# Kernel optimization log

Hardware: AMD Instinct MI355X
Metric: run time of the kernel (lower is better)

## Reference

```python
import jax, jax.numpy as jnp
import numpy as np

D_MODEL = 1024
N_HEADS = 16
HEAD_DIM = 64
SEQ = 2048
BATCH = 2
NEG = -1e9


def rotate_half(t):
    t1, t2 = jnp.split(t, 2, axis=-1)
    return jnp.concatenate([-t2, t1], axis=-1)


def setup_inputs() -> dict:
    key = jax.random.key(0)
    ks = jax.random.split(key, 7)
    std = 0.02
    x = jax.random.normal(ks[0], (BATCH, SEQ, D_MODEL), dtype=jnp.float32)
    # RoPE tables [seq_len, head_dim]
    inv_freq = 1.0 / (10000.0 ** (jnp.arange(0, HEAD_DIM, 2, dtype=jnp.float32) / HEAD_DIM))
    t = jnp.arange(SEQ, dtype=jnp.float32)
    freqs = jnp.outer(t, inv_freq)
    emb = jnp.concatenate([freqs, freqs], axis=-1)
    cos = jnp.cos(emb)
    sin = jnp.sin(emb)
    Wq = std * jax.random.normal(ks[1], (D_MODEL, D_MODEL), dtype=jnp.float32)
    Wk = std * jax.random.normal(ks[2], (D_MODEL, D_MODEL), dtype=jnp.float32)
    Wv = std * jax.random.normal(ks[3], (D_MODEL, D_MODEL), dtype=jnp.float32)
    Wo = std * jax.random.normal(ks[4], (D_MODEL, D_MODEL), dtype=jnp.float32)
    return {"x": x, "cos": cos, "sin": sin, "Wq": Wq, "Wk": Wk, "Wv": Wv, "Wo": Wo}


def reference(x, cos, sin, Wq, Wk, Wv, Wo):
    B, S, _ = x.shape
    scale = 1.0 / np.sqrt(HEAD_DIM)
    # projections (nn.Linear: y = x @ W.T)
    q = (x @ Wq.T).reshape(B, S, N_HEADS, HEAD_DIM).transpose(0, 2, 1, 3)  # [B,H,S,D]
    k = (x @ Wk.T).reshape(B, S, N_HEADS, HEAD_DIM).transpose(0, 2, 1, 3)
    v = (x @ Wv.T).reshape(B, S, N_HEADS, HEAD_DIM).transpose(0, 2, 1, 3)
    # RoPE
    c = cos[None, None, :, :]
    s = sin[None, None, :, :]
    q = q * c + rotate_half(q) * s
    k = k * c + rotate_half(k) * s
    # attention with additive causal mask
    scores = jnp.einsum('bhqd,bhkd->bhqk', q, k) * scale
    causal = jnp.triu(jnp.ones((S, S), dtype=jnp.float32), k=1) * NEG
    scores = scores + causal[None, None]
    attn = jax.nn.softmax(scores, axis=-1)
    out = jnp.einsum('bhqk,bhkd->bhqd', attn, v)
    out = out.transpose(0, 2, 1, 3).reshape(B, S, D_MODEL)
    return out @ Wo.T
```

## Files before the change

### kernel.cpp

```cpp
#include <hip/hip_runtime.h>
#include <hip/hip_bf16.h>
#include <math.h>

#define DM    1024
#define SEQL  2048
#define NB    2
#define MTOT  4096

typedef __attribute__((ext_vector_type(8))) short short8;
typedef __attribute__((ext_vector_type(4))) short short4v;
typedef __attribute__((ext_vector_type(4))) float float4v;

#define GLDS16(g, l) __builtin_amdgcn_global_load_lds( \
    (const __attribute__((address_space(1))) void*)(g), \
    (__attribute__((address_space(3))) void*)(l), 16, 0, 0)

__device__ __forceinline__ short f2bf(float f) {
  union { float f; unsigned u; } c; c.f = f;
  unsigned r = c.u + 0x7FFFu + ((c.u >> 16) & 1u);
  return (short)(r >> 16);
}

__device__ __forceinline__ int packbf(float a, float b) {
  union { float f; unsigned u; } ca, cb; ca.f = a; cb.f = b;
  return (int)__builtin_amdgcn_perm(cb.u + 0x8000u, ca.u + 0x8000u, 0x07060302u);
}

__global__ __launch_bounds__(256) void cvt_all(
    const float* __restrict__ x, const float* __restrict__ wq, const float* __restrict__ wk,
    const float* __restrict__ wv, const float* __restrict__ wo,
    short* __restrict__ xb, short* __restrict__ wqb, short* __restrict__ wkb,
    short* __restrict__ wvb, short* __restrict__ wob) {
  const int n4x = MTOT * DM / 4;
  int i = blockIdx.x * 256 + threadIdx.x;
  const float* s; short* d; int off;
  if (i < n4x) { s = x; d = xb; off = i; }
  else {
    int j = i - n4x;
    int sel = j >> 18;
    off = j & 0x3FFFF;
    s = (sel == 0) ? wq : (sel == 1) ? wk : (sel == 2) ? wv : wo;
    d = (sel == 0) ? wqb : (sel == 1) ? wkb : (sel == 2) ? wvb : wob;
  }
  float4 v = ((const float4*)s)[off];
  short4v o;
  o.x = f2bf(v.x); o.y = f2bf(v.y); o.z = f2bf(v.z); o.w = f2bf(v.w);
  ((short4v*)d)[off] = o;
}

__global__ __launch_bounds__(256, 3) void qkv_kernel(
    const short* __restrict__ A,
    const short* __restrict__ B0, const short* __restrict__ B1, const short* __restrict__ B2,
    short* __restrict__ out0, short* __restrict__ out1, short* __restrict__ out2,
    const float* __restrict__ cosp, const float* __restrict__ sinp)
{
  __shared__ short As[2][128 * 32];
  __shared__ short Bs[2][128 * 32];
  const int t = threadIdx.x;
  const int w = t >> 6, lane = t & 63;
  const int quad = lane >> 4, l16 = lane & 15;
  const int wm = w >> 1, wn = w & 1;
  const int bm = blockIdx.y * 128, bn = blockIdx.x * 128;

  const short* Bw = (blockIdx.z == 0) ? B0 : ((blockIdx.z == 1) ? B1 : B2);

  float4v acc[4][4];
#pragma unroll
  for (int i = 0; i < 4; ++i)
#pragma unroll
    for (int j = 0; j < 4; ++j) { float4v z = {0.f, 0.f, 0.f, 0.f}; acc[i][j] = z; }

  const int srow = t >> 2, skc = t & 3;
  auto stage = [&](int k0, int p) {
#pragma unroll
    for (int i = 0; i < 2; ++i) {
      const int row = (i * 256 + t) >> 2, kc = (i * 256 + t) & 3;
      GLDS16(A  + (size_t)(bm + row) * DM + k0 + kc * 8, &As[p][(i * 256 + w * 64) * 8]);
      GLDS16(Bw + (size_t)(bn + row) * DM + k0 + kc * 8, &Bs[p][(i * 256 + w * 64) * 8]);
    }
  };
  (void)srow; (void)skc;

  stage(0, 0);
  for (int ki = 0; ki < 32; ++ki) {
    const int p = ki & 1;
    __syncthreads();
    if (ki < 31) stage((ki + 1) * 32, p ^ 1);
    short8 af[4], bf[4];
#pragma unroll
    for (int mt = 0; mt < 4; ++mt) af[mt] = *(const short8*)&As[p][(wm * 64 + mt * 16 + l16) * 32 + quad * 8];
#pragma unroll
    for (int nt = 0; nt < 4; ++nt) bf[nt] = *(const short8*)&Bs[p][(wn * 64 + nt * 16 + l16) * 32 + quad * 8];
#pragma unroll
    for (int mt = 0; mt < 4; ++mt)
#pragma unroll
      for (int nt = 0; nt < 4; ++nt)
        acc[mt][nt] = __builtin_amdgcn_mfma_f32_16x16x32_bf16(af[mt], bf[nt], acc[mt][nt], 0, 0, 0);
  }

  if (blockIdx.z < 2) {
    short* qo = (blockIdx.z == 0) ? out0 : out1;
    const float sc = (blockIdx.z == 0) ? 0.18033688011112042f : 1.0f;
#pragma unroll
    for (int mt = 0; mt < 4; ++mt)
#pragma unroll
      for (int r = 0; r < 4; ++r) {
        int grow = bm + wm * 64 + mt * 16 + quad * 4 + r;
        int s = grow & (SEQL - 1);
        int base = grow * DM + bn + wn * 64;
#pragma unroll
        for (int nt = 0; nt < 2; ++nt) {
          int d1 = nt * 16 + l16;
          float q1 = acc[mt][nt][r], q2 = acc[mt][nt + 2][r];
          float c1 = cosp[s * 64 + d1] * sc,      s1 = sinp[s * 64 + d1] * sc;
          float c2 = cosp[s * 64 + 32 + d1] * sc, s2 = sinp[s * 64 + 32 + d1] * sc;
          qo[base + d1]      = f2bf(q1 * c1 - q2 * s1);
          qo[base + 32 + d1] = f2bf(q2 * c2 + q1 * s2);
        }
      }
  } else {
    short* vo = out2;
#pragma unroll
    for (int mt = 0; mt < 4; ++mt)
#pragma unroll
      for (int nt = 0; nt < 4; ++nt) {
        int gc = bn + wn * 64 + nt * 16 + l16;
        int g0 = bm + wm * 64 + mt * 16 + quad * 4;
        short4v pk;
#pragma unroll
        for (int r = 0; r < 4; ++r) pk[r] = f2bf(acc[mt][nt][r]);
        *(short4v*)&vo[(size_t)gc * MTOT + g0] = pk;
      }
  }
}

#if __has_builtin(__builtin_amdgcn_mfma_f32_16x16x16bf16_1k)
#define HAVE_MFMA16 1
#define MFMA16(a, b, c) __builtin_amdgcn_mfma_f32_16x16x16bf16_1k(a, b, c, 0, 0, 0)
#else
#define HAVE_MFMA16 0
#endif

__global__ __launch_bounds__(256, 2) void attn_kernel(
    const short* __restrict__ Q, const short* __restrict__ K,
    const short* __restrict__ Vt, short* __restrict__ O)
{
  __shared__ short Ks[2][128 * 64];
  __shared__ short Vs[2][64 * 128];
  const int t = threadIdx.x;
  const int w = t >> 6, lane = t & 63;
  const int quad = lane >> 4, l16 = lane & 15;
  const int qtA = blockIdx.x;
  const int qtB = 31 - blockIdx.x;
  const int bh = blockIdx.y;
  const int b = bh >> 4, h = bh & 15;
  const int rowbase = b * SEQL;
  const int colbase = h * 64;
  const int nktA = (qtA >> 1) + 1;
  const int nktB = (qtB >> 1) + 1;
  const int qA = qtA * 64 + w * 16 + l16;
  const int qB = qtB * 64 + w * 16 + l16;

  short8 aqA[2], aqB[2];
#pragma unroll
  for (int kk = 0; kk < 2; ++kk) {
    aqA[kk] = *(const short8*)&Q[(size_t)(rowbase + qA) * DM + colbase + kk * 32 + quad * 8];
    aqB[kk] = *(const short8*)&Q[(size_t)(rowbase + qB) * DM + colbase + kk * 32 + quad * 8];
  }

  float4v odA[4], odB[4];
#pragma unroll
  for (int j = 0; j < 4; ++j) { float4v z = {0.f, 0.f, 0.f, 0.f}; odA[j] = z; odB[j] = z; }
  float lA = 0.f, lB = 0.f;

  auto stage = [&](int kt, int p) {
    const short* Kbase = K + (size_t)(rowbase + kt * 128) * DM + colbase;
    const short* Vbase = Vt + (size_t)colbase * MTOT + rowbase + kt * 128;
    short* kd = &Ks[p][0];
    short* vd = &Vs[p][0];
#pragma unroll
    for (int j = 0; j < 4; ++j) {
      int i = j * 256 + t;
      int n = i >> 3, c = (i & 7) ^ (n & 7);
      GLDS16(Kbase + (size_t)n * DM + c * 8, kd + (j * 256 + w * 64) * 8);
    }
#pragma unroll
    for (int j = 0; j < 4; ++j) {
      int i = j * 256 + t;
      int d = i >> 4, c = (i & 15) ^ (d & 7);
      GLDS16(Vbase + (size_t)d * MTOT + c * 8, vd + (j * 256 + w * 64) * 8);
    }
  };

  stage(0, 0);
  for (int kt = 0; kt < nktB; ++kt) {
    const int p = kt & 1;
    __syncthreads();
    if (kt + 1 < nktB) stage(kt + 1, p ^ 1);
    const short* ks = &Ks[p][0];
    const short* vs = &Vs[p][0];
    const bool actA = (kt < nktA);
    const bool diagA = (kt == nktA - 1), diagB = (kt == nktB - 1);

    int pkA[8][2], pkB[8][2];
#pragma unroll
    for (int nt = 0; nt < 8; ++nt) {
      int n = nt * 16 + l16;
      short8 bk0 = *(const short8*)&ks[(n * 8 + (quad ^ (n & 7))) * 8];
      short8 bk1 = *(const short8*)&ks[(n * 8 + ((4 + quad) ^ (n & 7))) * 8];
      const int kb = kt * 128 + nt * 16 + quad * 4;
      float4v zz = {0.f, 0.f, 0.f, 0.f};
      float4v sB = __builtin_amdgcn_mfma_f32_16x16x32_bf16(bk0, aqB[0], zz, 0, 0, 0);
      sB = __builtin_amdgcn_mfma_f32_16x16x32_bf16(bk1, aqB[1], sB, 0, 0, 0);
      float pb[4];
#pragma unroll
      for (int r = 0; r < 4; ++r) {
        float pv = (diagB && (kb + r > qB)) ? 0.f : __builtin_amdgcn_exp2f(sB[r]);
        lB += pv; pb[r] = pv;
      }
      pkB[nt][0] = packbf(pb[0], pb[1]);
      pkB[nt][1] = packbf(pb[2], pb[3]);
      if (actA) {
        float4v sA = __builtin_amdgcn_mfma_f32_16x16x32_bf16(bk0, aqA[0], zz, 0, 0, 0);
        sA = __builtin_amdgcn_mfma_f32_16x16x32_bf16(bk1, aqA[1], sA, 0, 0, 0);
        float pa[4];
#pragma unroll
        for (int r = 0; r < 4; ++r) {
          float pv = (diagA && (kb + r > qA)) ? 0.f : __builtin_amdgcn_exp2f(sA[r]);
          lA += pv; pa[r] = pv;
        }
        pkA[nt][0] = packbf(pa[0], pa[1]);
        pkA[nt][1] = packbf(pa[2], pa[3]);
      }
    }

#if HAVE_MFMA16
#pragma unroll
    for (int kk = 0; kk < 8; ++kk) {
      union { int i[2]; short4v s; } ubB, ubA;
      ubB.i[0] = pkB[kk][0]; ubB.i[1] = pkB[kk][1];
      if (actA) { ubA.i[0] = pkA[kk][0]; ubA.i[1] = pkA[kk][1]; }
#pragma unroll
      for (int dt = 0; dt < 4; ++dt) {
        int d = dt * 16 + l16;
        short4v av = *(const short4v*)&vs[(d * 16 + ((kk * 2 + (quad >> 1)) ^ (d & 7))) * 8 + (quad & 1) * 4];
        odB[dt] = MFMA16(av, ubB.s, odB[dt]);
        if (actA) odA[dt] = MFMA16(av, ubA.s, odA[dt]);
      }
    }
#else
#pragma unroll
    for (int kk = 0; kk < 4; ++kk) {
      union { int i[4]; short8 s; } ubB, ubA;
#pragma unroll
      for (int dj = 0; dj < 4; ++dj) {
        int src = (((quad & 1) * 2 + (dj >> 1)) << 4) + l16;
        int b0 = __shfl(pkB[2 * kk][dj & 1], src);
        int b1 = __shfl(pkB[2 * kk + 1][dj & 1], src);
        ubB.i[dj] = (quad >= 2) ? b1 : b0;
        int a0 = __shfl(pkA[2 * kk][dj & 1], src);
        int a1 = __shfl(pkA[2 * kk + 1][dj & 1], src);
        ubA.i[dj] = (quad >= 2) ? a1 : a0;
      }
#pragma unroll
      for (int dt = 0; dt < 4; ++dt) {
        int d = dt * 16 + l16;
        short8 av = *(const short8*)&vs[(d * 16 + ((kk * 4 + quad) ^ (d & 7))) * 8];
        odB[dt] = __builtin_amdgcn_mfma_f32_16x16x32_bf16(av, ubB.s, odB[dt], 0, 0, 0);
        if (actA) odA[dt] = __builtin_amdgcn_mfma_f32_16x16x32_bf16(av, ubA.s, odA[dt], 0, 0, 0);
      }
    }
#endif
  }

  lA += __shfl_xor(lA, 16); lA += __shfl_xor(lA, 32);
  lB += __shfl_xor(lB, 16); lB += __shfl_xor(lB, 32);
  const float iA = 1.f / lA, iB = 1.f / lB;

#pragma unroll
  for (int dt = 0; dt < 4; ++dt) {
    short4v sa, sb;
#pragma unroll
    for (int r = 0; r < 4; ++r) { sa[r] = f2bf(odA[dt][r] * iA); sb[r] = f2bf(odB[dt][r] * iB); }
    int col = colbase + dt * 16 + quad * 4;
    *(short4v*)&O[(size_t)(rowbase + qA) * DM + col] = sa;
    *(short4v*)&O[(size_t)(rowbase + qB) * DM + col] = sb;
  }
}

__global__ __launch_bounds__(256, 2) void gemm_out(
    const short* __restrict__ A, const short* __restrict__ B,
    float* __restrict__ out)
{
  __shared__ short As[2][128 * 32];
  __shared__ short Bs[2][64 * 32];
  const int t = threadIdx.x;
  const int w = t >> 6, lane = t & 63;
  const int quad = lane >> 4, l16 = lane & 15;
  const int wm = w >> 1, wn = w & 1;
  const int bm = blockIdx.y * 128, bn = blockIdx.x * 64;

  float4v acc[4][2];
#pragma unroll
  for (int i = 0; i < 4; ++i)
#pragma unroll
    for (int j = 0; j < 2; ++j) { float4v z = {0.f, 0.f, 0.f, 0.f}; acc[i][j] = z; }

  auto stage = [&](int k0, int p) {
#pragma unroll
    for (int i = 0; i < 2; ++i) {
      const int row = (i * 256 + t) >> 2, kc = (i * 256 + t) & 3;
      GLDS16(A + (size_t)(bm + row) * DM + k0 + kc * 8, &As[p][(i * 256 + w * 64) * 8]);
    }
    {
      const int row = t >> 2, kc = t & 3;
      GLDS16(B + (size_t)(bn + row) * DM + k0 + kc * 8, &Bs[p][(w * 64) * 8]);
    }
  };

  stage(0, 0);
  for (int ki = 0; ki < 32; ++ki) {
    const int p = ki & 1;
    __syncthreads();
    if (ki < 31) stage((ki + 1) * 32, p ^ 1);
    short8 af[4], bf[2];
#pragma unroll
    for (int mt = 0; mt < 4; ++mt) af[mt] = *(const short8*)&As[p][(wm * 64 + mt * 16 + l16) * 32 + quad * 8];
#pragma unroll
    for (int nt = 0; nt < 2; ++nt) bf[nt] = *(const short8*)&Bs[p][(wn * 32 + nt * 16 + l16) * 32 + quad * 8];
#pragma unroll
    for (int mt = 0; mt < 4; ++mt)
#pragma unroll
      for (int nt = 0; nt < 2; ++nt)
        acc[mt][nt] = __builtin_amdgcn_mfma_f32_16x16x32_bf16(af[mt], bf[nt], acc[mt][nt], 0, 0, 0);
  }

#pragma unroll
  for (int mt = 0; mt < 4; ++mt)
#pragma unroll
    for (int nt = 0; nt < 2; ++nt)
#pragma unroll
      for (int r = 0; r < 4; ++r) {
        int grow = bm + wm * 64 + mt * 16 + quad * 4 + r;
        int gcol = bn + wn * 32 + nt * 16 + l16;
        out[(size_t)grow * DM + gcol] = acc[mt][nt][r];
      }
}

extern "C" void kernel_launch(void* const* d_in, const int* in_sizes, int n_in,
                              void* d_out, int out_size, void* d_ws, size_t ws_size,
                              hipStream_t stream) {
  const float* x    = (const float*)d_in[0];
  const float* cosp = (const float*)d_in[1];
  const float* sinp = (const float*)d_in[2];
  const float* Wq   = (const float*)d_in[3];
  const float* Wk   = (const float*)d_in[4];
  const float* Wv   = (const float*)d_in[5];
  const float* Wo   = (const float*)d_in[6];

  char* ws = (char*)d_ws;
  const size_t XB = (size_t)MTOT * DM * 2;
  const size_t WB = (size_t)DM * DM * 2;
  short* xb    = (short*)(ws);
  short* wqb   = (short*)(ws + XB);
  short* wkb   = (short*)(ws + XB + 1 * WB);
  short* wvb   = (short*)(ws + XB + 2 * WB);
  short* wob   = (short*)(ws + XB + 3 * WB);
  short* Qb    = (short*)(ws + XB + 4 * WB);
  short* Kb    = (short*)(ws + XB + 4 * WB + XB);
  short* Vtb   = (short*)(ws + XB + 4 * WB + 2 * XB);
  short* attnb = xb;

  const int n4tot = (MTOT * DM + 4 * DM * DM) / 4;
  hipLaunchKernelGGL(cvt_all, dim3(n4tot / 256), dim3(256), 0, stream,
                     x, Wq, Wk, Wv, Wo, xb, wqb, wkb, wvb, wob);

  hipLaunchKernelGGL(qkv_kernel, dim3(DM / 128, MTOT / 128, 3), dim3(256), 0, stream,
                     xb, wqb, wkb, wvb, Qb, Kb, Vtb, cosp, sinp);

  hipLaunchKernelGGL(attn_kernel, dim3(16, NB * 16), dim3(256), 0, stream,
                     Qb, Kb, Vtb, attnb);

  hipLaunchKernelGGL(gemm_out, dim3(DM / 64, MTOT / 128), dim3(256), 0, stream,
                     attnb, wob, (float*)d_out);
}
```

Before: 201.3 us.

## Split attention key tiles across two wave groups with LDS P staging and reduction

The attention kernel now runs 512 threads per block. Two groups of four waves each handle half of every 128-key tile, and their partial outputs and row sums are combined through shared memory at the end. The probability tile is written to LDS so the PV product can use 16x16x32 MFMA with P as the A operand, replacing the register-resident packing. K/V double buffering is dropped in favour of single-buffered loads with two barriers per iteration. This is meant to raise parallelism per block, at the cost of losing load/compute overlap, extra LDS traffic and scalar bf16 output stores.

```diff
diff --git a/kernel.cpp b/kernel.cpp
--- a/kernel.cpp
+++ b/kernel.cpp
@@ -70,7 +70,6 @@
 #pragma unroll
     for (int j = 0; j < 4; ++j) { float4v z = {0.f, 0.f, 0.f, 0.f}; acc[i][j] = z; }
 
-  const int srow = t >> 2, skc = t & 3;
   auto stage = [&](int k0, int p) {
 #pragma unroll
     for (int i = 0; i < 2; ++i) {
@@ -79,7 +78,6 @@
       GLDS16(Bw + (size_t)(bn + row) * DM + k0 + kc * 8, &Bs[p][(i * 256 + w * 64) * 8]);
     }
   };
-  (void)srow; (void)skc;
 
   stage(0, 0);
   for (int ki = 0; ki < 32; ++ki) {
@@ -134,32 +132,25 @@
   }
 }
 
-#if __has_builtin(__builtin_amdgcn_mfma_f32_16x16x16bf16_1k)
-#define HAVE_MFMA16 1
-#define MFMA16(a, b, c) __builtin_amdgcn_mfma_f32_16x16x16bf16_1k(a, b, c, 0, 0, 0)
-#else
-#define HAVE_MFMA16 0
-#endif
-
-__global__ __launch_bounds__(256, 2) void attn_kernel(
+__global__ __launch_bounds__(512, 4) void attn_kernel(
     const short* __restrict__ Q, const short* __restrict__ K,
     const short* __restrict__ Vt, short* __restrict__ O)
 {
-  __shared__ short Ks[2][128 * 64];
-  __shared__ short Vs[2][64 * 128];
+  __shared__ short smem[34816];
+  short* Ks = smem;
+  short* Vs = smem + 8192;
   const int t = threadIdx.x;
-  const int w = t >> 6, lane = t & 63;
+  const int wid = t >> 6, lane = t & 63;
   const int quad = lane >> 4, l16 = lane & 15;
-  const int qtA = blockIdx.x;
-  const int qtB = 31 - blockIdx.x;
-  const int bh = blockIdx.y;
-  const int b = bh >> 4, h = bh & 15;
-  const int rowbase = b * SEQL;
-  const int colbase = h * 64;
-  const int nktA = (qtA >> 1) + 1;
-  const int nktB = (qtB >> 1) + 1;
-  const int qA = qtA * 64 + w * 16 + l16;
-  const int qB = qtB * 64 + w * 16 + l16;
+  const int g = wid >> 2;
+  const int qg = wid & 3;
+  short* Pl = smem + 16384 + wid * (2 * 16 * 72);
+  const int qtA = blockIdx.x, qtB = 31 - blockIdx.x;
+  const int bh = blockIdx.y, b = bh >> 4, h = bh & 15;
+  const int rowbase = b * SEQL, colbase = h * 64;
+  const int nktA = (qtA >> 1) + 1, nktB = (qtB >> 1) + 1;
+  const int qA = qtA * 64 + qg * 16 + l16;
+  const int qB = qtB * 64 + qg * 16 + l16;
 
   short8 aqA[2], aqB[2];
 #pragma unroll
@@ -168,46 +159,38 @@
     aqB[kk] = *(const short8*)&Q[(size_t)(rowbase + qB) * DM + colbase + kk * 32 + quad * 8];
   }
 
-  float4v odA[4], odB[4];
-#pragma unroll
-  for (int j = 0; j < 4; ++j) { float4v z = {0.f, 0.f, 0.f, 0.f}; odA[j] = z; odB[j] = z; }
+  float4v oA[4], oB[4];
+#pragma unroll
+  for (int j = 0; j < 4; ++j) { float4v z = {0.f, 0.f, 0.f, 0.f}; oA[j] = z; oB[j] = z; }
   float lA = 0.f, lB = 0.f;
 
-  auto stage = [&](int kt, int p) {
-    const short* Kbase = K + (size_t)(rowbase + kt * 128) * DM + colbase;
-    const short* Vbase = Vt + (size_t)colbase * MTOT + rowbase + kt * 128;
-    short* kd = &Ks[p][0];
-    short* vd = &Vs[p][0];
-#pragma unroll
-    for (int j = 0; j < 4; ++j) {
-      int i = j * 256 + t;
-      int n = i >> 3, c = (i & 7) ^ (n & 7);
-      GLDS16(Kbase + (size_t)n * DM + c * 8, kd + (j * 256 + w * 64) * 8);
-    }
-#pragma unroll
-    for (int j = 0; j < 4; ++j) {
-      int i = j * 256 + t;
-      int d = i >> 4, c = (i & 15) ^ (d & 7);
-      GLDS16(Vbase + (size_t)d * MTOT + c * 8, vd + (j * 256 + w * 64) * 8);
-    }
-  };
-
-  stage(0, 0);
   for (int kt = 0; kt < nktB; ++kt) {
-    const int p = kt & 1;
+    {
+      const short* Kbase = K + (size_t)(rowbase + kt * 128) * DM + colbase;
+      const short* Vbase = Vt + (size_t)colbase * MTOT + rowbase + kt * 128;
+#pragma unroll
+      for (int j = 0; j < 2; ++j) {
+        int i = j * 512 + t;
+        int n = i >> 3, c = (i & 7) ^ (n & 7);
+        GLDS16(Kbase + (size_t)n * DM + c * 8, Ks + (j * 512 + wid * 64) * 8);
+      }
+#pragma unroll
+      for (int j = 0; j < 2; ++j) {
+        int i = j * 512 + t;
+        int d = i >> 4, c = (i & 15) ^ (d & 7);
+        GLDS16(Vbase + (size_t)d * MTOT + c * 8, Vs + (j * 512 + wid * 64) * 8);
+      }
+    }
     __syncthreads();
-    if (kt + 1 < nktB) stage(kt + 1, p ^ 1);
-    const short* ks = &Ks[p][0];
-    const short* vs = &Vs[p][0];
     const bool actA = (kt < nktA);
     const bool diagA = (kt == nktA - 1), diagB = (kt == nktB - 1);
 
-    int pkA[8][2], pkB[8][2];
-#pragma unroll
-    for (int nt = 0; nt < 8; ++nt) {
-      int n = nt * 16 + l16;
-      short8 bk0 = *(const short8*)&ks[(n * 8 + (quad ^ (n & 7))) * 8];
-      short8 bk1 = *(const short8*)&ks[(n * 8 + ((4 + quad) ^ (n & 7))) * 8];
+#pragma unroll
+    for (int ntl = 0; ntl < 4; ++ntl) {
+      const int nt = g * 4 + ntl;
+      const int n = nt * 16 + l16;
+      short8 bk0 = *(const short8*)&Ks[(n * 8 + (quad ^ (n & 7))) * 8];
+      short8 bk1 = *(const short8*)&Ks[(n * 8 + ((4 + quad) ^ (n & 7))) * 8];
       const int kb = kt * 128 + nt * 16 + quad * 4;
       float4v zz = {0.f, 0.f, 0.f, 0.f};
       float4v sB = __builtin_amdgcn_mfma_f32_16x16x32_bf16(bk0, aqB[0], zz, 0, 0, 0);
@@ -218,8 +201,8 @@
         float pv = (diagB && (kb + r > qB)) ? 0.f : __builtin_amdgcn_exp2f(sB[r]);
         lB += pv; pb[r] = pv;
       }
-      pkB[nt][0] = packbf(pb[0], pb[1]);
-      pkB[nt][1] = packbf(pb[2], pb[3]);
+      *(int2*)&Pl[1 * 16 * 72 + l16 * 72 + ntl * 16 + quad * 4] =
+          make_int2(packbf(pb[0], pb[1]), packbf(pb[2], pb[3]));
       if (actA) {
         float4v sA = __builtin_amdgcn_mfma_f32_16x16x32_bf16(bk0, aqA[0], zz, 0, 0, 0);
         sA = __builtin_amdgcn_mfma_f32_16x16x32_bf16(bk1, aqA[1], sA, 0, 0, 0);
@@ -229,62 +212,75 @@
           float pv = (diagA && (kb + r > qA)) ? 0.f : __builtin_amdgcn_exp2f(sA[r]);
           lA += pv; pa[r] = pv;
         }
-        pkA[nt][0] = packbf(pa[0], pa[1]);
-        pkA[nt][1] = packbf(pa[2], pa[3]);
-      }
-    }
-
-#if HAVE_MFMA16
-#pragma unroll
-    for (int kk = 0; kk < 8; ++kk) {
-      union { int i[2]; short4v s; } ubB, ubA;
-      ubB.i[0] = pkB[kk][0]; ubB.i[1] = pkB[kk][1];
-      if (actA) { ubA.i[0] = pkA[kk][0]; ubA.i[1] = pkA[kk][1]; }
+        *(int2*)&Pl[0 * 16 * 72 + l16 * 72 + ntl * 16 + quad * 4] =
+            make_int2(packbf(pa[0], pa[1]), packbf(pa[2], pa[3]));
+      }
+    }
+
+#pragma unroll
+    for (int kk = 0; kk < 2; ++kk) {
+      short8 apB = *(const short8*)&Pl[1 * 16 * 72 + l16 * 72 + kk * 32 + quad * 8];
+      short8 apA;
+      if (actA) apA = *(const short8*)&Pl[0 * 16 * 72 + l16 * 72 + kk * 32 + quad * 8];
+      const int c0 = g * 8 + kk * 4 + quad;
 #pragma unroll
       for (int dt = 0; dt < 4; ++dt) {
-        int d = dt * 16 + l16;
-        short4v av = *(const short4v*)&vs[(d * 16 + ((kk * 2 + (quad >> 1)) ^ (d & 7))) * 8 + (quad & 1) * 4];
-        odB[dt] = MFMA16(av, ubB.s, odB[dt]);
-        if (actA) odA[dt] = MFMA16(av, ubA.s, odA[dt]);
-      }
-    }
-#else
-#pragma unroll
-    for (int kk = 0; kk < 4; ++kk) {
-      union { int i[4]; short8 s; } ubB, ubA;
-#pragma unroll
-      for (int dj = 0; dj < 4; ++dj) {
-        int src = (((quad & 1) * 2 + (dj >> 1)) << 4) + l16;
-        int b0 = __shfl(pkB[2 * kk][dj & 1], src);
-        int b1 = __shfl(pkB[2 * kk + 1][dj & 1], src);
-        ubB.i[dj] = (quad >= 2) ? b1 : b0;
-        int a0 = __shfl(pkA[2 * kk][dj & 1], src);
-        int a1 = __shfl(pkA[2 * kk + 1][dj & 1], src);
-        ubA.i[dj] = (quad >= 2) ? a1 : a0;
-      }
-#pragma unroll
-      for (int dt = 0; dt < 4; ++dt) {
-        int d = dt * 16 + l16;
-        short8 av = *(const short8*)&vs[(d * 16 + ((kk * 4 + quad) ^ (d & 7))) * 8];
-        odB[dt] = __builtin_amdgcn_mfma_f32_16x16x32_bf16(av, ubB.s, odB[dt], 0, 0, 0);
-        if (actA) odA[dt] = __builtin_amdgcn_mfma_f32_16x16x32_bf16(av, ubA.s, odA[dt], 0, 0, 0);
-      }
-    }
-#endif
+        const int d = dt * 16 + l16;
+        short8 bv = *(const short8*)&Vs[(d * 16 + (c0 ^ (d & 7))) * 8];
+        oB[dt] = __builtin_amdgcn_mfma_f32_16x16x32_bf16(apB, bv, oB[dt], 0, 0, 0);
+        if (actA) oA[dt] = __builtin_amdgcn_mfma_f32_16x16x32_bf16(apA, bv, oA[dt], 0, 0, 0);
+      }
+    }
+    __syncthreads();
   }
 
   lA += __shfl_xor(lA, 16); lA += __shfl_xor(lA, 32);
   lB += __shfl_xor(lB, 16); lB += __shfl_xor(lB, 32);
-  const float iA = 1.f / lA, iB = 1.f / lB;
-
-#pragma unroll
-  for (int dt = 0; dt < 4; ++dt) {
-    short4v sa, sb;
-#pragma unroll
-    for (int r = 0; r < 4; ++r) { sa[r] = f2bf(odA[dt][r] * iA); sb[r] = f2bf(odB[dt][r] * iB); }
-    int col = colbase + dt * 16 + quad * 4;
-    *(short4v*)&O[(size_t)(rowbase + qA) * DM + col] = sa;
-    *(short4v*)&O[(size_t)(rowbase + qB) * DM + col] = sb;
+
+  __syncthreads();
+  float* Ored = (float*)smem;
+  float* Lred = (float*)smem + 8448;
+  if (g == 1) {
+#pragma unroll
+    for (int tile = 0; tile < 2; ++tile) {
+      const float4v* src = (tile == 0) ? oA : oB;
+      const int base = ((tile * 4 + qg) * 16) * 66;
+#pragma unroll
+      for (int dt = 0; dt < 4; ++dt)
+#pragma unroll
+        for (int r = 0; r < 4; ++r)
+          Ored[base + (quad * 4 + r) * 66 + dt * 16 + l16] = src[dt][r];
+    }
+    if (lane < 16) {
+      Lred[(0 * 4 + qg) * 16 + l16] = lA;
+      Lred[(1 * 4 + qg) * 16 + l16] = lB;
+    }
+  }
+  __syncthreads();
+  if (g == 0) {
+    const float tA = lA + Lred[(0 * 4 + qg) * 16 + l16];
+    const float tB = lB + Lred[(1 * 4 + qg) * 16 + l16];
+    float iAr[4], iBr[4];
+#pragma unroll
+    for (int r = 0; r < 4; ++r) {
+      iAr[r] = 1.f / __shfl(tA, quad * 4 + r);
+      iBr[r] = 1.f / __shfl(tB, quad * 4 + r);
+    }
+#pragma unroll
+    for (int tile = 0; tile < 2; ++tile) {
+      const float4v* src = (tile == 0) ? oA : oB;
+      const int qt = (tile == 0) ? qtA : qtB;
+      const int base = ((tile * 4 + qg) * 16) * 66;
+#pragma unroll
+      for (int dt = 0; dt < 4; ++dt)
+#pragma unroll
+        for (int r = 0; r < 4; ++r) {
+          float v = src[dt][r] + Ored[base + (quad * 4 + r) * 66 + dt * 16 + l16];
+          int grow = rowbase + qt * 64 + qg * 16 + quad * 4 + r;
+          int gcol = colbase + dt * 16 + l16;
+          O[(size_t)grow * DM + gcol] = f2bf(v * ((tile == 0) ? iAr[r] : iBr[r]));
+        }
+    }
   }
 }
 
@@ -378,7 +374,7 @@
   hipLaunchKernelGGL(qkv_kernel, dim3(DM / 128, MTOT / 128, 3), dim3(256), 0, stream,
                      xb, wqb, wkb, wvb, Qb, Kb, Vtb, cosp, sinp);
 
-  hipLaunchKernelGGL(attn_kernel, dim3(16, NB * 16), dim3(256), 0, stream,
+  hipLaunchKernelGGL(attn_kernel, dim3(16, NB * 16), dim3(512), 0, stream,
                      Qb, Kb, Vtb, attnb);
 
   hipLaunchKernelGGL(gemm_out, dim3(DM / 64, MTOT / 128), dim3(256), 0, stream,
```

After: 180.9 us (median of 2 runs). 1.11x faster.
